# Performance work log

Measured on AMD Instinct MI355X. Metric: run time of the kernel, lower is better.

Reference implementation:

```python
import jax, jax.numpy as jnp
import numpy as np

B, T, C = 4, 2048, 1024
T_PAST = 2048


def setup_inputs() -> dict:
    key = jax.random.key(0)
    ks = jax.random.split(key, 9)
    s = 1.0 / np.sqrt(C)
    return {
        "x": jax.random.normal(ks[0], (B, T, C), dtype=jnp.float32),
        "past_k": jax.random.normal(ks[1], (B, T_PAST, C), dtype=jnp.float32),
        "past_v": jax.random.normal(ks[2], (B, T_PAST, C), dtype=jnp.float32),
        "Wq": jax.random.normal(ks[3], (C, C), dtype=jnp.float32) * s,
        "bq": jnp.zeros((C,), dtype=jnp.float32),
        "Wk": jax.random.normal(ks[4], (C, C), dtype=jnp.float32) * s,
        "bk": jnp.zeros((C,), dtype=jnp.float32),
        "Wv": jax.random.normal(ks[5], (C, C), dtype=jnp.float32) * s,
        "bv": jnp.zeros((C,), dtype=jnp.float32),
    }


def reference(x, past_k, past_v, Wq, bq, Wk, bk, Wv, bv):
    Bb, Tt, Cc = x.shape
    # nn.Linear: y = x @ W^T + b
    Q = jnp.einsum('btc,dc->btd', x, Wq) + bq
    K = jnp.einsum('btc,dc->btd', x, Wk) + bk
    V = jnp.einsum('btc,dc->btd', x, Wv) + bv
    K = jnp.concatenate([past_k, K], axis=1)
    V = jnp.concatenate([past_v, V], axis=1)
    T_total = K.shape[1]
    scores = jnp.einsum('btc,bsc->bts', Q, K) / jnp.sqrt(jnp.float32(Cc))
    # Faithful to torch.tril(ones(T, T_total)): allow j <= i (even across cache)
    mask = jnp.arange(T_total)[None, :] <= jnp.arange(Tt)[:, None]
    scores = jnp.where(mask[None, :, :], scores, -jnp.inf)
    weights = jax.nn.softmax(scores, axis=-1)
    out = jnp.einsum('bts,bsc->btc', weights, V)
    return (out, K, V)
```

## Files before the change

### kernel.cpp

```cpp
#include <hip/hip_runtime.h>


typedef __bf16 bf16x8 __attribute__((ext_vector_type(8)));
typedef float f32x4 __attribute__((ext_vector_type(4)));

#define BB   4
#define TQ   2048
#define CD   1024
#define TPAST 2048
#define TTOT 4096
#define MROWS (BB * TQ)
#define SSTRIDE_FALLBACK ((size_t)TTOT * CD * 2)
#define SLOTU 8192

__device__ __forceinline__ unsigned short f32_to_bf16u(float f) {
  unsigned int u = __float_as_uint(f);
  u += 0x7FFFu + ((u >> 16) & 1u);
  return (unsigned short)(u >> 16);
}
__device__ __forceinline__ float bf16u_to_f32(unsigned short h) {
  unsigned int u = ((unsigned int)h) << 16;
  return __uint_as_float(u);
}
__device__ __forceinline__ unsigned int pack_bf16(float a, float b) {
  return (unsigned int)f32_to_bf16u(a) | ((unsigned int)f32_to_bf16u(b) << 16);
}

__device__ __forceinline__ void gload_lds16(const unsigned short* g,
                                            unsigned short* l) {
  __builtin_amdgcn_global_load_lds(
      (const __attribute__((address_space(1))) void*)g,
      (__attribute__((address_space(3))) void*)l, 16, 0, 0);
}

struct StagePtrs { const unsigned short *a0, *a1, *b0, *b1; };

__device__ __forceinline__ void stage_step(StagePtrs& p, unsigned short* lds,
                                           int stOff, int wv) {
  unsigned short* base = lds + stOff + wv * 512;
  gload_lds16(p.a0, base);
  gload_lds16(p.a1, base + 2048);
  gload_lds16(p.b0, base + 4096);
  gload_lds16(p.b1, base + 6144);
  p.a0 += 32; p.a1 += 32; p.b0 += 32; p.b1 += 32;
}

__device__ __forceinline__ void gemm_core_v2(
    StagePtrs p, unsigned short* lds, int NT,
    int wr, int wc, int lane, int wv, f32x4 acc[4][4]) {
  const int gph8 = (((lane >> 4) ^ (lane & 3))) * 8;
  const int aRd = (wr * 64 + (lane & 15)) * 32 + gph8;
  const int bRd = 4096 + (wc * 64 + (lane & 15)) * 32 + gph8;
  stage_step(p, lds, 0, wv);
  stage_step(p, lds, SLOTU, wv);
  int stOff = 2 * SLOTU;
  int rdOff = 0;
  for (int t = 0; t < NT; ++t) {
    if (t + 2 < NT) {
      stage_step(p, lds, stOff, wv);
      stOff = (stOff == 2 * SLOTU) ? 0 : stOff + SLOTU;
    }
    const int rem = NT - 1 - t;
    if (rem >= 2)      asm volatile("s_waitcnt vmcnt(8)" ::: "memory");
    else if (rem == 1) asm volatile("s_waitcnt vmcnt(4)" ::: "memory");
    else               asm volatile("s_waitcnt vmcnt(0)" ::: "memory");
    asm volatile("s_barrier" ::: "memory");
    bf16x8 af[4], bg[4];
#pragma unroll
    for (int i = 0; i < 4; ++i)
      af[i] = *(const bf16x8*)&lds[rdOff + aRd + i * 512];
#pragma unroll
    for (int i = 0; i < 4; ++i)
      bg[i] = *(const bf16x8*)&lds[rdOff + bRd + i * 512];
    asm volatile("s_waitcnt lgkmcnt(0)" ::: "memory");
    __builtin_amdgcn_sched_barrier(0);
    asm volatile("s_barrier" ::: "memory");
    __builtin_amdgcn_s_setprio(1);
#pragma unroll
    for (int mi = 0; mi < 4; ++mi)
#pragma unroll
      for (int ni = 0; ni < 4; ++ni)
        acc[mi][ni] = __builtin_amdgcn_mfma_f32_16x16x32_bf16(
            af[mi], bg[ni], acc[mi][ni], 0, 0, 0);
    __builtin_amdgcn_s_setprio(0);
    rdOff = (rdOff == 2 * SLOTU) ? 0 : rdOff + SLOTU;
  }
}

__device__ __forceinline__ const unsigned short* swz_src(
    const unsigned short* base, size_t rowStart, size_t ld,
    int part, int wv, int lane) {
  int row = part * 64 + wv * 16 + (lane >> 2);
  int gp = (lane & 3) ^ ((lane >> 2) & 3);
  return base + (rowStart + row) * ld + gp * 8;
}

#define TP_PAD 134
#define VCT_BLOCKS 2048
#define R0_END 2097152
#define R1_END 2359296
#define R2_END 2621440
#define R3_END 2883584
#define R4_END 4980736
__global__ __launch_bounds__(256) void prep(
    const float* __restrict__ x, const float* __restrict__ wq,
    const float* __restrict__ wk, const float* __restrict__ wv,
    const float* __restrict__ pk, const float* __restrict__ pV,
    unsigned short* __restrict__ xb, unsigned short* __restrict__ wqb,
    unsigned short* __restrict__ wkb, unsigned short* __restrict__ wvb,
    unsigned short* __restrict__ kb,
    float* __restrict__ outV, unsigned short* __restrict__ VT,
    float* __restrict__ outKcopy) {
  const int tid = threadIdx.x;
  if (blockIdx.x < VCT_BLOCKS) {
    __shared__ unsigned short T[32 * TP_PAD];
    const int bid = blockIdx.x;
    const int s0 = (bid & 63) * 32, c0 = ((bid >> 6) & 7) * 128, b = bid >> 9;
    const int s = tid >> 3, i8 = tid & 7;
    const float* src = &pV[(size_t)(b * TPAST + s0 + s) * CD + c0];
    float* dst = &outV[(size_t)b * (TTOT * CD) + (size_t)(s0 + s) * CD + c0];
#pragma unroll
    for (int k = 0; k < 4; ++k) {
      int c = k * 32 + i8 * 4;
      float4 f = *(const float4*)&src[c];
      *(float4*)&dst[c] = f;
      *(unsigned int*)&T[s * TP_PAD + c]     = pack_bf16(f.x, f.y);
      *(unsigned int*)&T[s * TP_PAD + c + 2] = pack_bf16(f.z, f.w);
    }
    __syncthreads();
    const int c = tid >> 2, sq = tid & 3;
#pragma unroll
    for (int ii = 0; ii < 2; ++ii) {
      int cc = c + ii * 64;
      unsigned short tmp[8];
#pragma unroll
      for (int j = 0; j < 8; ++j) tmp[j] = T[(sq * 8 + j) * TP_PAD + cc];
      *(uint4*)&VT[(size_t)(b * CD + c0 + cc) * TPAST + s0 + sq * 8] = *(uint4*)tmp;
    }
    return;
  }
  int i = (blockIdx.x - VCT_BLOCKS) * 256 + tid;
  const float* src; unsigned short* dst; int off;
  bool isPk = false;
  if (i < R0_END)      { src = x;  dst = xb;  off = i; }
  else if (i < R1_END) { src = wq; dst = wqb; off = i - R0_END; }
  else if (i < R2_END) { src = wk; dst = wkb; off = i - R1_END; }
  else if (i < R3_END) { src = wv; dst = wvb; off = i - R2_END; }
  else                 { src = pk; dst = kb;  off = i - R3_END; isPk = true; }
  float4 f = ((const float4*)src)[off];
  uint2 o;
  o.x = pack_bf16(f.x, f.y);
  o.y = pack_bf16(f.z, f.w);
  ((uint2*)dst)[off] = o;
  if (isPk && outKcopy) {
    int b = off >> 19;
    int rem = off & 524287;
    ((float4*)outKcopy)[(size_t)b * 1048576 + rem] = f;
  }
}

__global__ __launch_bounds__(256) void copy_past_kernel(
    const float* __restrict__ src, float* __restrict__ dst) {
  int i = blockIdx.x * 256 + threadIdx.x;
  int b = i >> 19;
  int rem = i & 524287;
  ((float4*)dst)[(size_t)b * 1048576 + rem] = ((const float4*)src)[i];
}

__global__ __launch_bounds__(256, 3) void proj_qkv(
    const unsigned short* __restrict__ A,
    const unsigned short* __restrict__ Wq_,
    const unsigned short* __restrict__ Wv_,
    const unsigned short* __restrict__ Wk_,
    const float* __restrict__ bq_, const float* __restrict__ bv_,
    const float* __restrict__ bk_,
    unsigned short* __restrict__ outQ,
    float* __restrict__ outV, float* __restrict__ outK) {
  __shared__ unsigned short lds[3 * SLOTU];
  const int tm = blockIdx.x * 128;
  const int which = blockIdx.y >> 3;
  const int tn = (blockIdx.y & 7) * 128;
  const unsigned short* W = (which == 0) ? Wq_ : (which == 1) ? Wv_ : Wk_;
  const float* bias = (which == 0) ? bq_ : (which == 1) ? bv_ : bk_;
  const int tid = threadIdx.x, lane = tid & 63, wv = tid >> 6;
  const int wr = wv >> 1, wc = wv & 1;
  StagePtrs p;
  p.a0 = swz_src(A, tm, CD, 0, wv, lane);
  p.a1 = swz_src(A, tm, CD, 1, wv, lane);
  p.b0 = swz_src(W, tn, CD, 0, wv, lane);
  p.b1 = swz_src(W, tn, CD, 1, wv, lane);
  f32x4 acc[4][4] = {};
  gemm_core_v2(p, lds, CD / 32, wr, wc, lane, wv, acc);
  const int rsub = (lane >> 4) * 4, csub = lane & 15;
#pragma unroll
  for (int mi = 0; mi < 4; ++mi)
#pragma unroll
    for (int ni = 0; ni < 4; ++ni) {
      int gcn = tn + wc * 64 + ni * 16 + csub;
      float bvv = bias[gcn];
#pragma unroll
      for (int r = 0; r < 4; ++r) {
        int grw = tm + wr * 64 + mi * 16 + rsub + r;
        float v = acc[mi][ni][r] + bvv;
        if (which == 0) {
          outQ[(size_t)grw * CD + gcn] = f32_to_bf16u(v * 0.03125f);
        } else {
          int b = grw >> 11, t = grw & (TQ - 1);
          float* o = (which == 1) ? outV : outK;
          o[(size_t)b * (TTOT * CD) + (size_t)(TPAST + t) * CD + gcn] = v;
        }
      }
    }
}

__global__ __launch_bounds__(256, 3) void score_gemm(
    const unsigned short* __restrict__ Q,
    const unsigned short* __restrict__ KB,
    unsigned short* __restrict__ S16, size_t sstride,
    float* __restrict__ l_part) {
  const int t0 = blockIdx.x * 128, s0 = blockIdx.y * 128, b = blockIdx.z;
  if (s0 > t0) return;
  __shared__ unsigned short lds[3 * SLOTU];
  __shared__ float lpart[128][2];
  const int tid = threadIdx.x, lane = tid & 63, wv = tid >> 6;
  const int wr = wv >> 1, wc = wv & 1;
  StagePtrs p;
  p.a0 = swz_src(Q, (size_t)b * TQ + t0, CD, 0, wv, lane);
  p.a1 = swz_src(Q, (size_t)b * TQ + t0, CD, 1, wv, lane);
  p.b0 = swz_src(KB, (size_t)b * TPAST + s0, CD, 0, wv, lane);
  p.b1 = swz_src(KB, (size_t)b * TPAST + s0, CD, 1, wv, lane);
  f32x4 acc[4][4] = {};
  gemm_core_v2(p, lds, CD / 32, wr, wc, lane, wv, acc);
  const int rsub = (lane >> 4) * 4, csub = lane & 15;
  float rsum[4][4];
#pragma unroll
  for (int mi = 0; mi < 4; ++mi)
#pragma unroll
    for (int r = 0; r < 4; ++r) rsum[mi][r] = 0.f;
#pragma unroll
  for (int mi = 0; mi < 4; ++mi)
#pragma unroll
    for (int ni = 0; ni < 4; ++ni) {
      int gs = s0 + wc * 64 + ni * 16 + csub;
#pragma unroll
      for (int r = 0; r < 4; ++r) {
        int gt = t0 + wr * 64 + mi * 16 + rsub + r;
        float e = (gs <= gt) ? __expf(acc[mi][ni][r] - 16.f) : 0.f;
        unsigned short h = f32_to_bf16u(e);
        S16[(size_t)b * sstride + (size_t)gt * TPAST + gs] = h;
        rsum[mi][r] += bf16u_to_f32(h);
      }
    }
#pragma unroll
  for (int mi = 0; mi < 4; ++mi)
#pragma unroll
    for (int r = 0; r < 4; ++r) {
      float v = rsum[mi][r];
      v += __shfl_xor(v, 1);
      v += __shfl_xor(v, 2);
      v += __shfl_xor(v, 4);
      v += __shfl_xor(v, 8);
      rsum[mi][r] = v;
    }
  if ((lane & 15) == 0) {
#pragma unroll
    for (int mi = 0; mi < 4; ++mi)
#pragma unroll
      for (int r = 0; r < 4; ++r)
        lpart[wr * 64 + mi * 16 + rsub + r][wc] = rsum[mi][r];
  }
  __syncthreads();
  if (tid < 128)
    l_part[((size_t)b * TQ + t0 + tid) * 16 + (s0 >> 7)] =
        lpart[tid][0] + lpart[tid][1];
}

__global__ __launch_bounds__(256, 3) void pv_gemm(
    const unsigned short* __restrict__ Pb,
    const unsigned short* __restrict__ VT,
    float* __restrict__ O, size_t sstride,
    const float* __restrict__ l_part) {
  const int t0 = blockIdx.x * 128, c0 = blockIdx.y * 128, b = blockIdx.z;
  __shared__ unsigned short lds[3 * SLOTU];
  const int tid = threadIdx.x, lane = tid & 63, wv = tid >> 6;
  const int wr = wv >> 1, wc = wv & 1;
  StagePtrs p;
  p.a0 = swz_src(Pb + (size_t)b * sstride, t0, TPAST, 0, wv, lane);
  p.a1 = swz_src(Pb + (size_t)b * sstride, t0, TPAST, 1, wv, lane);
  p.b0 = swz_src(VT, (size_t)b * CD + c0, TPAST, 0, wv, lane);
  p.b1 = swz_src(VT, (size_t)b * CD + c0, TPAST, 1, wv, lane);
  f32x4 acc[4][4] = {};
  const int s_end = (t0 + 128 < TPAST) ? (t0 + 128) : TPAST;
  gemm_core_v2(p, lds, s_end / 32, wr, wc, lane, wv, acc);
  __syncthreads();
  float* linv = (float*)lds;
  if (tid < 128) {
    const float* lp = &l_part[((size_t)b * TQ + t0 + tid) * 16];
    float s = 0.f;
    const int nj = (t0 >> 7) + 1;
    for (int j = 0; j < nj; ++j) s += lp[j];
    linv[tid] = 1.0f / s;
  }
  __syncthreads();
  const int rsub = (lane >> 4) * 4, csub = lane & 15;
#pragma unroll
  for (int mi = 0; mi < 4; ++mi)
#pragma unroll
    for (int ni = 0; ni < 4; ++ni) {
      int gcn = c0 + wc * 64 + ni * 16 + csub;
#pragma unroll
      for (int r = 0; r < 4; ++r) {
        int lrow = wr * 64 + mi * 16 + rsub + r;
        int gt = t0 + lrow;
        O[(size_t)(b * TQ + gt) * CD + gcn] = acc[mi][ni][r] * linv[lrow];
      }
    }
}

extern "C" void kernel_launch(void* const* d_in, const int* in_sizes, int n_in,
                              void* d_out, int out_size, void* d_ws, size_t ws_size,
                              hipStream_t stream) {
  const float* x  = (const float*)d_in[0];
  const float* pk = (const float*)d_in[1];
  const float* pv = (const float*)d_in[2];
  const float* Wq = (const float*)d_in[3];
  const float* bq = (const float*)d_in[4];
  const float* Wk = (const float*)d_in[5];
  const float* bk = (const float*)d_in[6];
  const float* Wv = (const float*)d_in[7];
  const float* bv = (const float*)d_in[8];

  float* out  = (float*)d_out;
  float* outK = out + (size_t)BB * TQ * CD;
  float* outV = outK + (size_t)BB * TTOT * CD;

  unsigned short* xb  = (unsigned short*)d_ws;
  unsigned short* wqb = xb + (size_t)MROWS * CD;
  unsigned short* wkb = wqb + (size_t)CD * CD;
  unsigned short* wvb = wkb + (size_t)CD * CD;
  unsigned short* qb  = wvb + (size_t)CD * CD;
  unsigned short* vtb = qb + (size_t)MROWS * CD;
  unsigned short* kb  = vtb + (size_t)BB * CD * TPAST;
  unsigned short* wsEnd = kb + (size_t)BB * TPAST * CD;

  const size_t baseBytes = (size_t)((char*)wsEnd - (char*)d_ws);
  const size_t s16Bytes  = (size_t)BB * TQ * TPAST * 2;
  const size_t lpBytes   = (size_t)BB * TQ * 16 * 4;
  const bool fit = ws_size >= baseBytes + s16Bytes + lpBytes;

  unsigned short* S16;
  float* l_part;
  size_t sstride;
  if (fit) {
    S16 = wsEnd;
    l_part = (float*)(S16 + (size_t)BB * TQ * TPAST);
    sstride = (size_t)TQ * TPAST;
  } else {
    S16 = (unsigned short*)outK;
    l_part = (float*)wsEnd;
    sstride = SSTRIDE_FALLBACK;
  }

  prep<<<VCT_BLOCKS + R4_END / 256, 256, 0, stream>>>(
      x, Wq, Wk, Wv, pk, pv, xb, wqb, wkb, wvb, kb, outV, vtb,
      fit ? outK : nullptr);
  proj_qkv<<<dim3(MROWS / 128, 24), 256, 0, stream>>>(
      xb, wqb, wvb, wkb, bq, bv, bk, qb, outV, outK);
  score_gemm<<<dim3(TQ / 128, TPAST / 128, BB), 256, 0, stream>>>(
      qb, kb, S16, sstride, l_part);
  pv_gemm<<<dim3(TQ / 128, CD / 128, BB), 256, 0, stream>>>(
      S16, vtb, out, sstride, l_part);
  if (!fit)
    copy_past_kernel<<<BB * TPAST * CD / 4 / 256, 256, 0, stream>>>(pk, outK);
}
```

Baseline: 209.4 us.

## Fuse past-K/V conversion and transpose into the QKV projection kernel

Splits the prep kernel so only the x/weight bf16 conversion runs first. The memory-bound past_v transpose/copy and past_k conversion/copy now run as extra blocks interleaved (8 per 3 GEMM tiles) inside the projection GEMM launch. The aim is to overlap bandwidth-heavy copies with compute-bound MFMA tiles and drop a serial pass over past K/V. In exchange, the copy blocks share the GEMM kernel's launch bounds and LDS allocation, which may lower occupancy or disturb the GEMM tile scheduling.

```diff
diff --git a/kernel.cpp b/kernel.cpp
--- a/kernel.cpp
+++ b/kernel.cpp
@@ -95,68 +95,26 @@
   return base + (rowStart + row) * ld + gp * 8;
 }
 
-#define TP_PAD 134
-#define VCT_BLOCKS 2048
 #define R0_END 2097152
 #define R1_END 2359296
 #define R2_END 2621440
 #define R3_END 2883584
-#define R4_END 4980736
-__global__ __launch_bounds__(256) void prep(
+__global__ __launch_bounds__(256) void prep_a(
     const float* __restrict__ x, const float* __restrict__ wq,
     const float* __restrict__ wk, const float* __restrict__ wv,
-    const float* __restrict__ pk, const float* __restrict__ pV,
     unsigned short* __restrict__ xb, unsigned short* __restrict__ wqb,
-    unsigned short* __restrict__ wkb, unsigned short* __restrict__ wvb,
-    unsigned short* __restrict__ kb,
-    float* __restrict__ outV, unsigned short* __restrict__ VT,
-    float* __restrict__ outKcopy) {
-  const int tid = threadIdx.x;
-  if (blockIdx.x < VCT_BLOCKS) {
-    __shared__ unsigned short T[32 * TP_PAD];
-    const int bid = blockIdx.x;
-    const int s0 = (bid & 63) * 32, c0 = ((bid >> 6) & 7) * 128, b = bid >> 9;
-    const int s = tid >> 3, i8 = tid & 7;
-    const float* src = &pV[(size_t)(b * TPAST + s0 + s) * CD + c0];
-    float* dst = &outV[(size_t)b * (TTOT * CD) + (size_t)(s0 + s) * CD + c0];
-#pragma unroll
-    for (int k = 0; k < 4; ++k) {
-      int c = k * 32 + i8 * 4;
-      float4 f = *(const float4*)&src[c];
-      *(float4*)&dst[c] = f;
-      *(unsigned int*)&T[s * TP_PAD + c]     = pack_bf16(f.x, f.y);
-      *(unsigned int*)&T[s * TP_PAD + c + 2] = pack_bf16(f.z, f.w);
-    }
-    __syncthreads();
-    const int c = tid >> 2, sq = tid & 3;
-#pragma unroll
-    for (int ii = 0; ii < 2; ++ii) {
-      int cc = c + ii * 64;
-      unsigned short tmp[8];
-#pragma unroll
-      for (int j = 0; j < 8; ++j) tmp[j] = T[(sq * 8 + j) * TP_PAD + cc];
-      *(uint4*)&VT[(size_t)(b * CD + c0 + cc) * TPAST + s0 + sq * 8] = *(uint4*)tmp;
-    }
-    return;
-  }
-  int i = (blockIdx.x - VCT_BLOCKS) * 256 + tid;
+    unsigned short* __restrict__ wkb, unsigned short* __restrict__ wvb) {
+  int i = blockIdx.x * 256 + threadIdx.x;
   const float* src; unsigned short* dst; int off;
-  bool isPk = false;
   if (i < R0_END)      { src = x;  dst = xb;  off = i; }
   else if (i < R1_END) { src = wq; dst = wqb; off = i - R0_END; }
   else if (i < R2_END) { src = wk; dst = wkb; off = i - R1_END; }
-  else if (i < R3_END) { src = wv; dst = wvb; off = i - R2_END; }
-  else                 { src = pk; dst = kb;  off = i - R3_END; isPk = true; }
+  else                 { src = wv; dst = wvb; off = i - R2_END; }
   float4 f = ((const float4*)src)[off];
   uint2 o;
   o.x = pack_bf16(f.x, f.y);
   o.y = pack_bf16(f.z, f.w);
   ((uint2*)dst)[off] = o;
-  if (isPk && outKcopy) {
-    int b = off >> 19;
-    int rem = off & 524287;
-    ((float4*)outKcopy)[(size_t)b * 1048576 + rem] = f;
-  }
 }
 
 __global__ __launch_bounds__(256) void copy_past_kernel(
@@ -167,7 +125,9 @@
   ((float4*)dst)[(size_t)b * 1048576 + rem] = ((const float4*)src)[i];
 }
 
-__global__ __launch_bounds__(256, 3) void proj_qkv(
+#define TP_PAD 134
+#define VCT_BLOCKS 2048
+__global__ __launch_bounds__(256, 3) void proj_fused(
     const unsigned short* __restrict__ A,
     const unsigned short* __restrict__ Wq_,
     const unsigned short* __restrict__ Wv_,
@@ -175,14 +135,69 @@
     const float* __restrict__ bq_, const float* __restrict__ bv_,
     const float* __restrict__ bk_,
     unsigned short* __restrict__ outQ,
-    float* __restrict__ outV, float* __restrict__ outK) {
+    float* __restrict__ outV, float* __restrict__ outK,
+    const float* __restrict__ pk, const float* __restrict__ pV,
+    unsigned short* __restrict__ kb, unsigned short* __restrict__ VT,
+    float* __restrict__ outKcopy) {
   __shared__ unsigned short lds[3 * SLOTU];
-  const int tm = blockIdx.x * 128;
-  const int which = blockIdx.y >> 3;
-  const int tn = (blockIdx.y & 7) * 128;
+  const int grp = blockIdx.x / 11, slot = blockIdx.x % 11;
+  const int tid = threadIdx.x;
+
+  if (slot >= 3) {
+    const int midx = grp * 8 + (slot - 3);
+    if (midx < VCT_BLOCKS) {
+      unsigned short* T = lds;
+      const int s0 = (midx & 63) * 32, c0 = ((midx >> 6) & 7) * 128,
+                b = midx >> 9;
+      const int s = tid >> 3, i8 = tid & 7;
+      const float* src = &pV[(size_t)(b * TPAST + s0 + s) * CD + c0];
+      float* dst = &outV[(size_t)b * (TTOT * CD) + (size_t)(s0 + s) * CD + c0];
+#pragma unroll
+      for (int k = 0; k < 4; ++k) {
+        int c = k * 32 + i8 * 4;
+        float4 f = *(const float4*)&src[c];
+        *(float4*)&dst[c] = f;
+        *(unsigned int*)&T[s * TP_PAD + c]     = pack_bf16(f.x, f.y);
+        *(unsigned int*)&T[s * TP_PAD + c + 2] = pack_bf16(f.z, f.w);
+      }
+      __syncthreads();
+      const int c = tid >> 2, sq = tid & 3;
+#pragma unroll
+      for (int ii = 0; ii < 2; ++ii) {
+        int cc = c + ii * 64;
+        unsigned short tmp[8];
+#pragma unroll
+        for (int j = 0; j < 8; ++j) tmp[j] = T[(sq * 8 + j) * TP_PAD + cc];
+        *(uint4*)&VT[(size_t)(b * CD + c0 + cc) * TPAST + s0 + sq * 8] =
+            *(uint4*)tmp;
+      }
+    } else {
+      const int idx = midx - VCT_BLOCKS;
+#pragma unroll
+      for (int j = 0; j < 4; ++j) {
+        int off = idx * 1024 + j * 256 + tid;
+        float4 f = ((const float4*)pk)[off];
+        uint2 o;
+        o.x = pack_bf16(f.x, f.y);
+        o.y = pack_bf16(f.z, f.w);
+        ((uint2*)kb)[off] = o;
+        if (outKcopy) {
+          int b = off >> 19, rem = off & 524287;
+          ((float4*)outKcopy)[(size_t)b * 1048576 + rem] = f;
+        }
+      }
+    }
+    return;
+  }
+
+  const int gi = grp * 3 + slot;
+  const int tm = (gi & 63) * 128;
+  const int yy = gi >> 6;
+  const int which = yy >> 3;
+  const int tn = (yy & 7) * 128;
   const unsigned short* W = (which == 0) ? Wq_ : (which == 1) ? Wv_ : Wk_;
   const float* bias = (which == 0) ? bq_ : (which == 1) ? bv_ : bk_;
-  const int tid = threadIdx.x, lane = tid & 63, wv = tid >> 6;
+  const int lane = tid & 63, wv = tid >> 6;
   const int wr = wv >> 1, wc = wv & 1;
   StagePtrs p;
   p.a0 = swz_src(A, tm, CD, 0, wv, lane);
@@ -361,11 +376,10 @@
     sstride = SSTRIDE_FALLBACK;
   }
 
-  prep<<<VCT_BLOCKS + R4_END / 256, 256, 0, stream>>>(
-      x, Wq, Wk, Wv, pk, pv, xb, wqb, wkb, wvb, kb, outV, vtb,
-      fit ? outK : nullptr);
-  proj_qkv<<<dim3(MROWS / 128, 24), 256, 0, stream>>>(
-      xb, wqb, wvb, wkb, bq, bv, bk, qb, outV, outK);
+  prep_a<<<R3_END / 256, 256, 0, stream>>>(x, Wq, Wk, Wv, xb, wqb, wkb, wvb);
+  proj_fused<<<512 * 11, 256, 0, stream>>>(
+      xb, wqb, wvb, wkb, bq, bv, bk, qb, outV, outK,
+      pk, pv, kb, vtb, fit ? outK : nullptr);
   score_gemm<<<dim3(TQ / 128, TPAST / 128, BB), 256, 0, stream>>>(
       qb, kb, S16, sstride, l_part);
   pv_gemm<<<dim3(TQ / 128, CD / 128, BB), 256, 0, stream>>>(
```

Result: slower. 218.2 us (+4.2%).

## Widen QKV projection tile to 128x256 with double-buffered LDS pipeline

Applied to the files above, without the earlier changes.

The QKV projection GEMM now uses a 128x256 output tile per block, so each warp computes 64x128 with a 4x8 MFMA accumulator grid. Staging is double-buffered instead of triple-buffered, and the grid's y dimension is halved. Each A tile load now feeds twice as many output columns, which cuts global and LDS traffic per FLOP. The costs are more accumulator registers, occupancy lowered from 3 to 2 blocks, and fewer blocks to fill the GPU.

```diff
diff --git a/kernel.cpp b/kernel.cpp
--- a/kernel.cpp
+++ b/kernel.cpp
@@ -12,6 +12,7 @@
 #define MROWS (BB * TQ)
 #define SSTRIDE_FALLBACK ((size_t)TTOT * CD * 2)
 #define SLOTU 8192
+#define WSLOT 12288
 
 __device__ __forceinline__ unsigned short f32_to_bf16u(float f) {
   unsigned int u = __float_as_uint(f);
@@ -31,6 +32,14 @@
   __builtin_amdgcn_global_load_lds(
       (const __attribute__((address_space(1))) void*)g,
       (__attribute__((address_space(3))) void*)l, 16, 0, 0);
+}
+
+__device__ __forceinline__ const unsigned short* swz_src(
+    const unsigned short* base, size_t rowStart, size_t ld,
+    int part, int wv, int lane) {
+  int row = part * 64 + wv * 16 + (lane >> 2);
+  int gp = (lane & 3) ^ ((lane >> 2) & 3);
+  return base + (rowStart + row) * ld + gp * 8;
 }
 
 struct StagePtrs { const unsigned short *a0, *a1, *b0, *b1; };
@@ -87,12 +96,56 @@
   }
 }
 
-__device__ __forceinline__ const unsigned short* swz_src(
-    const unsigned short* base, size_t rowStart, size_t ld,
-    int part, int wv, int lane) {
-  int row = part * 64 + wv * 16 + (lane >> 2);
-  int gp = (lane & 3) ^ ((lane >> 2) & 3);
-  return base + (rowStart + row) * ld + gp * 8;
+struct StageW { const unsigned short *a0, *a1, *b0, *b1, *b2, *b3; };
+
+__device__ __forceinline__ void stage_w(StageW& p, unsigned short* lds,
+                                        int stOff, int wv) {
+  unsigned short* base = lds + stOff + wv * 512;
+  gload_lds16(p.a0, base);
+  gload_lds16(p.a1, base + 2048);
+  gload_lds16(p.b0, base + 4096);
+  gload_lds16(p.b1, base + 6144);
+  gload_lds16(p.b2, base + 8192);
+  gload_lds16(p.b3, base + 10240);
+  p.a0 += 32; p.a1 += 32; p.b0 += 32; p.b1 += 32; p.b2 += 32; p.b3 += 32;
+}
+
+__device__ __forceinline__ void gemm_core_w(
+    StageW p, unsigned short* lds, int NT,
+    int wr, int wc, int lane, int wv, f32x4 acc[4][8]) {
+  const int gph8 = (((lane >> 4) ^ (lane & 3))) * 8;
+  const int aRd = (wr * 64 + (lane & 15)) * 32 + gph8;
+  const int bRd = 4096 + (wc * 128 + (lane & 15)) * 32 + gph8;
+  stage_w(p, lds, 0, wv);
+  int stOff = WSLOT, rdOff = 0;
+  for (int t = 0; t < NT; ++t) {
+    if (t + 1 < NT) {
+      stage_w(p, lds, stOff, wv);
+      stOff ^= WSLOT;
+    }
+    if (t + 1 < NT) asm volatile("s_waitcnt vmcnt(6)" ::: "memory");
+    else            asm volatile("s_waitcnt vmcnt(0)" ::: "memory");
+    asm volatile("s_barrier" ::: "memory");
+    bf16x8 af[4], bg[8];
+#pragma unroll
+    for (int i = 0; i < 4; ++i)
+      af[i] = *(const bf16x8*)&lds[rdOff + aRd + i * 512];
+#pragma unroll
+    for (int i = 0; i < 8; ++i)
+      bg[i] = *(const bf16x8*)&lds[rdOff + bRd + i * 512];
+    asm volatile("s_waitcnt lgkmcnt(0)" ::: "memory");
+    __builtin_amdgcn_sched_barrier(0);
+    asm volatile("s_barrier" ::: "memory");
+    __builtin_amdgcn_s_setprio(1);
+#pragma unroll
+    for (int mi = 0; mi < 4; ++mi)
+#pragma unroll
+      for (int ni = 0; ni < 8; ++ni)
+        acc[mi][ni] = __builtin_amdgcn_mfma_f32_16x16x32_bf16(
+            af[mi], bg[ni], acc[mi][ni], 0, 0, 0);
+    __builtin_amdgcn_s_setprio(0);
+    rdOff ^= WSLOT;
+  }
 }
 
 #define TP_PAD 134
@@ -167,7 +220,7 @@
   ((float4*)dst)[(size_t)b * 1048576 + rem] = ((const float4*)src)[i];
 }
 
-__global__ __launch_bounds__(256, 3) void proj_qkv(
+__global__ __launch_bounds__(256, 2) void proj_qkv(
     const unsigned short* __restrict__ A,
     const unsigned short* __restrict__ Wq_,
     const unsigned short* __restrict__ Wv_,
@@ -176,27 +229,29 @@
     const float* __restrict__ bk_,
     unsigned short* __restrict__ outQ,
     float* __restrict__ outV, float* __restrict__ outK) {
-  __shared__ unsigned short lds[3 * SLOTU];
+  __shared__ unsigned short lds[2 * WSLOT];
   const int tm = blockIdx.x * 128;
-  const int which = blockIdx.y >> 3;
-  const int tn = (blockIdx.y & 7) * 128;
+  const int which = blockIdx.y >> 2;
+  const int tn = (blockIdx.y & 3) * 256;
   const unsigned short* W = (which == 0) ? Wq_ : (which == 1) ? Wv_ : Wk_;
   const float* bias = (which == 0) ? bq_ : (which == 1) ? bv_ : bk_;
   const int tid = threadIdx.x, lane = tid & 63, wv = tid >> 6;
   const int wr = wv >> 1, wc = wv & 1;
-  StagePtrs p;
+  StageW p;
   p.a0 = swz_src(A, tm, CD, 0, wv, lane);
   p.a1 = swz_src(A, tm, CD, 1, wv, lane);
   p.b0 = swz_src(W, tn, CD, 0, wv, lane);
   p.b1 = swz_src(W, tn, CD, 1, wv, lane);
-  f32x4 acc[4][4] = {};
-  gemm_core_v2(p, lds, CD / 32, wr, wc, lane, wv, acc);
+  p.b2 = swz_src(W, tn, CD, 2, wv, lane);
+  p.b3 = swz_src(W, tn, CD, 3, wv, lane);
+  f32x4 acc[4][8] = {};
+  gemm_core_w(p, lds, CD / 32, wr, wc, lane, wv, acc);
   const int rsub = (lane >> 4) * 4, csub = lane & 15;
 #pragma unroll
   for (int mi = 0; mi < 4; ++mi)
 #pragma unroll
-    for (int ni = 0; ni < 4; ++ni) {
-      int gcn = tn + wc * 64 + ni * 16 + csub;
+    for (int ni = 0; ni < 8; ++ni) {
+      int gcn = tn + wc * 128 + ni * 16 + csub;
       float bvv = bias[gcn];
 #pragma unroll
       for (int r = 0; r < 4; ++r) {
@@ -364,7 +419,7 @@
   prep<<<VCT_BLOCKS + R4_END / 256, 256, 0, stream>>>(
       x, Wq, Wk, Wv, pk, pv, xb, wqb, wkb, wvb, kb, outV, vtb,
       fit ? outK : nullptr);
-  proj_qkv<<<dim3(MROWS / 128, 24), 256, 0, stream>>>(
+  proj_qkv<<<dim3(MROWS / 128, 12), 256, 0, stream>>>(
       xb, wqb, wvb, wkb, bq, bv, bk, qb, outV, outK);
   score_gemm<<<dim3(TQ / 128, TPAST / 128, BB), 256, 0, stream>>>(
       qb, kb, S16, sstride, l_part);
```

Result: no change. 211.1 us (+0.8%).
